# Performance work log

Hardware: AMD Instinct MI355X
Metric: run time of the kernel (lower is better)

## Reference

```python
import jax, jax.numpy as jnp
import numpy as np

B, L, C, H = 256, 200, 4, 128


def setup_inputs() -> dict:
    key = jax.random.key(0)
    ks = jax.random.split(key, 6)
    seqs = jax.random.normal(ks[0], (B, L, C, H), dtype=jnp.float32)
    # valid prefix of random length, padding (True) at the tail
    lengths = jax.random.randint(ks[1], (B,), 1, L + 1)
    timeline_mask = (jnp.arange(L)[None, :] >= lengths[:, None])[:, :, None]  # [B,L,1] bool
    attention_mask = jnp.zeros((L, L), dtype=bool)  # unused by the module
    s = 1.0 / np.sqrt(H)  # torch GRU default init U(-1/sqrt(H), 1/sqrt(H))
    W_ih = jax.random.uniform(ks[2], (C, 3 * H, H), minval=-s, maxval=s, dtype=jnp.float32)
    W_hh = jax.random.uniform(ks[3], (C, 3 * H, H), minval=-s, maxval=s, dtype=jnp.float32)
    b_ih = jax.random.uniform(ks[4], (C, 3 * H), minval=-s, maxval=s, dtype=jnp.float32)
    b_hh = jax.random.uniform(ks[5], (C, 3 * H), minval=-s, maxval=s, dtype=jnp.float32)
    return {"seqs": seqs, "timeline_mask": timeline_mask, "attention_mask": attention_mask,
            "W_ih": W_ih, "W_hh": W_hh, "b_ih": b_ih, "b_hh": b_hh}


def batched_roll(x, shifts):
    # x: [B, L, H]; per-sample circular shift along time (torch.roll semantics)
    Ldim = x.shape[1]
    idx = (jnp.arange(Ldim)[None, :] - shifts[:, None]) % Ldim  # [B, L]
    return jnp.take_along_axis(x, idx[:, :, None], axis=1)


def gru(x, W_ih, W_hh, b_ih, b_hh):
    # single-layer batch_first GRU, h0 = 0 (torch nn.GRU math)
    xp = jnp.einsum('blh,gh->blg', x, W_ih) + b_ih  # [B, L, 3H] input projections
    Hd = W_hh.shape[1]

    def step(h, xt):
        gh = h @ W_hh.T + b_hh
        i_r, i_z, i_n = jnp.split(xt, 3, axis=-1)
        h_r, h_z, h_n = jnp.split(gh, 3, axis=-1)
        r = jax.nn.sigmoid(i_r + h_r)
        z = jax.nn.sigmoid(i_z + h_z)
        n = jnp.tanh(i_n + r * h_n)
        h_new = (1.0 - z) * n + z * h
        return h_new, h_new

    h0 = jnp.zeros((x.shape[0], Hd), x.dtype)
    _, ys = jax.lax.scan(step, h0, jnp.swapaxes(xp, 0, 1))  # scan over time
    return jnp.swapaxes(ys, 0, 1)  # [B, L, H]


def reference(seqs, timeline_mask, attention_mask, W_ih, W_hh, b_ih, b_hh):
    mask = timeline_mask[:, :, 0]                 # [B, L] True = pad
    length = jnp.sum(~mask, axis=1)               # count of valid steps
    zero_length = jnp.sum(mask, axis=1)           # count of padded steps
    outs = []
    for i in range(seqs.shape[2]):                # loop over C experts (distinct weights)
        x = batched_roll(seqs[:, :, i, :], length)
        y = gru(x, W_ih[i], W_hh[i], b_ih[i], b_hh[i])
        y = batched_roll(y, zero_length)
        y = jnp.where(timeline_mask, 0.0, y)      # masked_fill(timeline_mask, 0.0)
        outs.append(y)
    return jnp.stack(outs, axis=0)  # [C, B, L, H] (list of experts in the original)
```

## Files before the change

### kernel.cpp

```cpp
#include <hip/hip_runtime.h>
#include <hip/hip_bf16.h>

#define BB 256
#define LL 200
#define CC 4
#define HH 128
#define G3 384

typedef short bf16x8 __attribute__((ext_vector_type(8)));
typedef float f32x4 __attribute__((ext_vector_type(4)));

#define MFMA16(a, b, c) __builtin_amdgcn_mfma_f32_16x16x32_bf16((a), (b), (c), 0, 0, 0)

__device__ __forceinline__ short bf16_rne(float x) {
    union { float f; unsigned u; } v; v.f = x;
    unsigned r = v.u + 0x7FFFu + ((v.u >> 16) & 1u);
    return (short)(r >> 16);
}
__device__ __forceinline__ float rcp_(float x) { return __builtin_amdgcn_rcpf(x); }
__device__ __forceinline__ float sigm_(float x) { return rcp_(1.0f + __expf(-x)); }
__device__ __forceinline__ float tanhf_(float x) { return 2.0f * rcp_(1.0f + __expf(-2.0f * x)) - 1.0f; }

__device__ __forceinline__ unsigned cvtpk(float lo, float hi) {
    unsigned r;
    asm("v_cvt_pk_bf16_f32 %0, %1, %2" : "=v"(r) : "v"(lo), "v"(hi));
    return r;
}
__device__ __forceinline__ uint2 pack4(float4 v) {
    uint2 p;
    p.x = cvtpk(v.x, v.y);
    p.y = cvtpk(v.z, v.w);
    return p;
}

__global__ void compute_lens_kernel(const unsigned char* __restrict__ mask8,
                                    int* __restrict__ lens) {
    __shared__ int bad;
    int b = threadIdx.x;
    if (b == 0) bad = 0;
    __syncthreads();
    int cnt8 = 0, prev = 0, mono = 1;
    for (int t = 0; t < LL; ++t) {
        int v = mask8[b * LL + t] ? 1 : 0;
        cnt8 += (v == 0);
        if (v < prev) mono = 0;
        prev = v;
    }
    if (!mono) atomicAdd(&bad, 1);
    __syncthreads();
    int len;
    if (bad == 0) {
        len = cnt8;
    } else {
        const int* m32 = (const int*)mask8;
        int c = 0;
        for (int t = 0; t < LL; ++t) c += (m32[b * LL + t] == 0);
        len = c;
    }
    if (len < 1) len = 1;
    if (len > LL) len = LL;
    lens[b] = len;
}

__global__ void wsplit_kernel(const float* __restrict__ Wih, const float* __restrict__ Whh,
                              short* __restrict__ wih_hi, short* __restrict__ whh_hi) {
    int i = blockIdx.x * 256 + threadIdx.x;
    wih_hi[i] = bf16_rne(Wih[i]);
    whh_hi[i] = bf16_rne(Whh[i]);
}

__global__ __launch_bounds__(512, 2) void gru_fused_kernel(
    const float* __restrict__ seqs,
    const int*   __restrict__ lens,
    const short* __restrict__ wih_hi,
    const short* __restrict__ whh_hi,
    const float* __restrict__ b_ih,
    const float* __restrict__ b_hh,
    float*       __restrict__ out)
{
    const int bt = blockIdx.x;
    const int c  = blockIdx.y;
    const int bbase = bt * 16;
    const int tid = threadIdx.x;
    const int w = tid >> 6;
    const int l = tid & 63;
    const int l15 = l & 15, g = l >> 4;

    __shared__ __align__(16) short hA[2][4][512];
    __shared__ __align__(16) short xs[2][4][512];

    bf16x8 BH[3][4], WI[3][4];
    #pragma unroll
    for (int q = 0; q < 3; ++q) {
        const int NT = q * 8 + w;
        #pragma unroll
        for (int ks = 0; ks < 4; ++ks) {
            size_t off = (size_t)(c * G3 + NT * 16 + l15) * HH + ks * 32 + g * 8;
            BH[q][ks] = *(const bf16x8*)(whh_hi + off);
            WI[q][ks] = *(const bf16x8*)(wih_hi + off);
        }
    }

    const int col0 = w * 16 + l15;
    const int ksw = w >> 1;
    const int hwbase = (((w & 1) * 2 + (l15 >> 3)) * 16 + g * 4) * 8 + (l15 & 7);

    const int bsl = tid >> 5;
    const int k0s = (tid & 31) * 4;
    const int ksx = k0s >> 5;
    const int xwbase = ((((k0s >> 3) & 3) * 16 + bsl) * 8 + (k0s & 7));
    const int lenS = lens[bbase + bsl];
    const float* srow0 = seqs + ((size_t)(bbase + bsl) * LL * CC + c) * HH + k0s;
    int ts0 = LL - lenS;
    int ts1 = ts0 + 1; if (ts1 >= LL) ts1 -= LL;
    float4 xr0 = *(const float4*)(srow0 + (size_t)ts0 * (CC * HH));
    float4 xr1 = *(const float4*)(srow0 + (size_t)ts1 * (CC * HH));
    int txs = ts1 + 1; if (txs >= LL) txs -= LL;
    const float* xptr = srow0 + (size_t)txs * (CC * HH);
    const ptrdiff_t xstep = CC * HH;
    const ptrdiff_t xwrap = (ptrdiff_t)(LL - 1) * CC * HH;

    const float bRs = b_hh[c * G3 + col0]       + b_ih[c * G3 + col0];
    const float bZs = b_hh[c * G3 + 128 + col0] + b_ih[c * G3 + 128 + col0];
    const float bHN = b_hh[c * G3 + 256 + col0];
    const float bIN = b_ih[c * G3 + 256 + col0];
    const f32x4 cZZ  = (f32x4){0.f, 0.f, 0.f, 0.f};
    const f32x4 cHN4 = (f32x4){bHN, bHN, bHN, bHN};
    const f32x4 cR4  = (f32x4){bRs, bRs, bRs, bRs};
    const f32x4 cZ4  = (f32x4){bZs, bZs, bZs, bZs};
    const f32x4 cN4  = (f32x4){bIN, bIN, bIN, bIN};

    int lenr[4], tcur[4];
    float* optr[4];
    #pragma unroll
    for (int r = 0; r < 4; ++r) {
        lenr[r] = lens[bbase + g * 4 + r];
        tcur[r] = LL - lenr[r];
        optr[r] = out + ((size_t)(c * BB + bbase + g * 4 + r) * LL + tcur[r]) * HH + col0;
    }
    const ptrdiff_t owrap = (ptrdiff_t)(LL - 1) * HH;
    float hold[4] = { 0.f, 0.f, 0.f, 0.f };

    for (int i = tid; i < 1024; i += 512) ((int*)hA[0])[i] = 0;

    *(uint2*)&xs[0][ksx][xwbase] = pack4(xr0);
    *(uint2*)&xs[1][ksx][xwbase] = pack4(xr1);
    __syncthreads();

    f32x4 xacc[3];
    {
        bf16x8 xh0 = *(const bf16x8*)&xs[0][0][l * 8];
        xacc[0] = MFMA16(xh0, WI[0][0], cR4);
        xacc[1] = MFMA16(xh0, WI[1][0], cZ4);
        xacc[2] = MFMA16(xh0, WI[2][0], cN4);
        #pragma unroll
        for (int ks = 1; ks < 4; ++ks) {
            bf16x8 xh = *(const bf16x8*)&xs[0][ks][l * 8];
            #pragma unroll
            for (int q = 0; q < 3; ++q)
                xacc[q] = MFMA16(xh, WI[q][ks], xacc[q]);
        }
    }
    float4 xraw = *(const float4*)xptr;
    txs = (txs + 1 == LL) ? 0 : txs + 1;
    xptr = (txs == 0) ? xptr - xwrap : xptr + xstep;

    __syncthreads();

#define STEP_BODY(HB, HN)                                                      \
    {                                                                          \
        f32x4 racc[3];                                                         \
        {                                                                      \
            bf16x8 ah0 = *(const bf16x8*)&hA[HB][0][l * 8];                    \
            racc[0] = MFMA16(ah0, BH[0][0], cZZ);                              \
            racc[1] = MFMA16(ah0, BH[1][0], cZZ);                              \
            racc[2] = MFMA16(ah0, BH[2][0], cHN4);                             \
            _Pragma("unroll")                                                  \
            for (int ks = 1; ks < 4; ++ks) {                                   \
                bf16x8 ah = *(const bf16x8*)&hA[HB][ks][l * 8];                \
                _Pragma("unroll")                                              \
                for (int q = 0; q < 3; ++q)                                    \
                    racc[q] = MFMA16(ah, BH[q][ks], racc[q]);                  \
            }                                                                  \
        }                                                                      \
        float hnew[4];                                                         \
        _Pragma("unroll")                                                      \
        for (int r = 0; r < 4; ++r) {                                          \
            float gr = sigm_(racc[0][r] + xacc[0][r]);                         \
            float gz = sigm_(racc[1][r] + xacc[1][r]);                         \
            float gn = tanhf_(xacc[2][r] + gr * racc[2][r]);                   \
            float hv = gn + gz * (hold[r] - gn);                               \
            hnew[r] = hv;                                                      \
            hold[r] = hv;                                                      \
        }                                                                      \
        {                                                                      \
            unsigned pk01 = cvtpk(hold[0], hold[1]);                           \
            unsigned pk23 = cvtpk(hold[2], hold[3]);                           \
            hA[HN][ksw][hwbase]      = (short)(pk01 & 0xffffu);                \
            hA[HN][ksw][hwbase + 8]  = (short)(pk01 >> 16);                    \
            hA[HN][ksw][hwbase + 16] = (short)(pk23 & 0xffffu);                \
            hA[HN][ksw][hwbase + 24] = (short)(pk23 >> 16);                    \
        }                                                                      \
        _Pragma("unroll")                                                      \
        for (int r = 0; r < 4; ++r) {                                          \
            int t = tcur[r];                                                   \
            *optr[r] = (t < lenr[r]) ? hnew[r] : 0.0f;                         \
            int wrapped = (t + 1 == LL);                                       \
            tcur[r] = wrapped ? 0 : t + 1;                                     \
            optr[r] = wrapped ? optr[r] - owrap : optr[r] + HH;                \
        }                                                                      \
        {                                                                      \
            bf16x8 xh0 = *(const bf16x8*)&xs[HN][0][l * 8];                    \
            xacc[0] = MFMA16(xh0, WI[0][0], cR4);                              \
            xacc[1] = MFMA16(xh0, WI[1][0], cZ4);                              \
            xacc[2] = MFMA16(xh0, WI[2][0], cN4);                              \
            _Pragma("unroll")                                                  \
            for (int ks = 1; ks < 4; ++ks) {                                   \
                bf16x8 xh = *(const bf16x8*)&xs[HN][ks][l * 8];                \
                _Pragma("unroll")                                              \
                for (int q = 0; q < 3; ++q)                                    \
                    xacc[q] = MFMA16(xh, WI[q][ks], xacc[q]);                  \
            }                                                                  \
        }                                                                      \
        *(uint2*)&xs[HB][ksx][xwbase] = pack4(xraw);                           \
        xraw = *(const float4*)xptr;                                           \
        txs = (txs + 1 == LL) ? 0 : txs + 1;                                   \
        xptr = (txs == 0) ? xptr - xwrap : xptr + xstep;                       \
        asm volatile("s_waitcnt lgkmcnt(0)" ::: "memory");                     \
        __builtin_amdgcn_s_barrier();                                          \
        __builtin_amdgcn_sched_barrier(0);                                     \
    }

    for (int si2 = 0; si2 < LL; si2 += 2) {
        STEP_BODY(0, 1)
        STEP_BODY(1, 0)
    }
#undef STEP_BODY
}

extern "C" void kernel_launch(void* const* d_in, const int* in_sizes, int n_in,
                              void* d_out, int out_size, void* d_ws, size_t ws_size,
                              hipStream_t stream) {
    const float* seqs  = (const float*)d_in[0];
    const unsigned char* tmask = (const unsigned char*)d_in[1];
    const float* W_ih  = (const float*)d_in[3];
    const float* W_hh  = (const float*)d_in[4];
    const float* b_ih  = (const float*)d_in[5];
    const float* b_hh  = (const float*)d_in[6];
    float* out = (float*)d_out;

    char* ws = (char*)d_ws;
    int*   lens   = (int*)(ws);
    short* wih_hi = (short*)(ws + 1024);
    short* whh_hi = (short*)(ws + 1024 + 393216);

    compute_lens_kernel<<<1, BB, 0, stream>>>(tmask, lens);
    wsplit_kernel<<<768, 256, 0, stream>>>(W_ih, W_hh, wih_hi, whh_hi);

    gru_fused_kernel<<<dim3(16, CC), 512, 0, stream>>>(
        seqs, lens, wih_hi, whh_hi, b_ih, b_hh, out);
}
```

Measured before the change: 202.7 us.

## Transpose MFMA operands so each lane owns 4 hidden dims, vectorize stores

Swaps the MFMA A/B operands so the accumulator holds 4 consecutive hidden dimensions for one batch row per lane, rather than 4 batch rows for one dimension. The hidden state and inputs are now kept in LDS as row-major [batch][padded 136] arrays. With this layout the per-step hidden write becomes a single 8-byte LDS store instead of four 2-byte stores, and the output write becomes one float4 global store with a single length/pointer state per lane. The intent is fewer LDS and global store instructions and more coalesced output writes, at the cost of a different LDS bank-access pattern for the strided bf16x8 reads.

Result: faster. 179.8 us (-11.3%).

```diff
diff --git a/kernel.cpp b/kernel.cpp
--- a/kernel.cpp
+++ b/kernel.cpp
@@ -6,6 +6,7 @@
 #define CC 4
 #define HH 128
 #define G3 384
+#define XP 136
 
 typedef short bf16x8 __attribute__((ext_vector_type(8)));
 typedef float f32x4 __attribute__((ext_vector_type(4)));
@@ -86,8 +87,8 @@
     const int l = tid & 63;
     const int l15 = l & 15, g = l >> 4;
 
-    __shared__ __align__(16) short hA[2][4][512];
-    __shared__ __align__(16) short xs[2][4][512];
+    __shared__ __align__(16) short hA[2][16][XP];
+    __shared__ __align__(16) short xs[2][16][XP];
 
     bf16x8 BH[3][4], WI[3][4];
     #pragma unroll
@@ -101,14 +102,32 @@
         }
     }
 
-    const int col0 = w * 16 + l15;
-    const int ksw = w >> 1;
-    const int hwbase = (((w & 1) * 2 + (l15 >> 3)) * 16 + g * 4) * 8 + (l15 & 7);
+    const int dim0 = w * 16 + g * 4;
+
+    f32x4 cR4, cZ4, cHN4, cN4;
+    {
+        float4 rh = *(const float4*)(b_hh + c * G3 + dim0);
+        float4 ri = *(const float4*)(b_ih + c * G3 + dim0);
+        float4 zh = *(const float4*)(b_hh + c * G3 + 128 + dim0);
+        float4 zi = *(const float4*)(b_ih + c * G3 + 128 + dim0);
+        float4 nh = *(const float4*)(b_hh + c * G3 + 256 + dim0);
+        float4 ni = *(const float4*)(b_ih + c * G3 + 256 + dim0);
+        cR4  = (f32x4){rh.x + ri.x, rh.y + ri.y, rh.z + ri.z, rh.w + ri.w};
+        cZ4  = (f32x4){zh.x + zi.x, zh.y + zi.y, zh.z + zi.z, zh.w + zi.w};
+        cHN4 = (f32x4){nh.x, nh.y, nh.z, nh.w};
+        cN4  = (f32x4){ni.x, ni.y, ni.z, ni.w};
+    }
+    const f32x4 cZZ = (f32x4){0.f, 0.f, 0.f, 0.f};
+
+    const int bme = bbase + l15;
+    const int lenb = lens[bme];
+    int tcur = LL - lenb;
+    float* optr = out + ((size_t)(c * BB + bme) * LL + tcur) * HH + dim0;
+    const ptrdiff_t owrap = (ptrdiff_t)(LL - 1) * HH;
+    float hold[4] = { 0.f, 0.f, 0.f, 0.f };
 
     const int bsl = tid >> 5;
     const int k0s = (tid & 31) * 4;
-    const int ksx = k0s >> 5;
-    const int xwbase = ((((k0s >> 3) & 3) * 16 + bsl) * 8 + (k0s & 7));
     const int lenS = lens[bbase + bsl];
     const float* srow0 = seqs + ((size_t)(bbase + bsl) * LL * CC + c) * HH + k0s;
     int ts0 = LL - lenS;
@@ -120,45 +139,24 @@
     const ptrdiff_t xstep = CC * HH;
     const ptrdiff_t xwrap = (ptrdiff_t)(LL - 1) * CC * HH;
 
-    const float bRs = b_hh[c * G3 + col0]       + b_ih[c * G3 + col0];
-    const float bZs = b_hh[c * G3 + 128 + col0] + b_ih[c * G3 + 128 + col0];
-    const float bHN = b_hh[c * G3 + 256 + col0];
-    const float bIN = b_ih[c * G3 + 256 + col0];
-    const f32x4 cZZ  = (f32x4){0.f, 0.f, 0.f, 0.f};
-    const f32x4 cHN4 = (f32x4){bHN, bHN, bHN, bHN};
-    const f32x4 cR4  = (f32x4){bRs, bRs, bRs, bRs};
-    const f32x4 cZ4  = (f32x4){bZs, bZs, bZs, bZs};
-    const f32x4 cN4  = (f32x4){bIN, bIN, bIN, bIN};
-
-    int lenr[4], tcur[4];
-    float* optr[4];
-    #pragma unroll
-    for (int r = 0; r < 4; ++r) {
-        lenr[r] = lens[bbase + g * 4 + r];
-        tcur[r] = LL - lenr[r];
-        optr[r] = out + ((size_t)(c * BB + bbase + g * 4 + r) * LL + tcur[r]) * HH + col0;
-    }
-    const ptrdiff_t owrap = (ptrdiff_t)(LL - 1) * HH;
-    float hold[4] = { 0.f, 0.f, 0.f, 0.f };
-
-    for (int i = tid; i < 1024; i += 512) ((int*)hA[0])[i] = 0;
-
-    *(uint2*)&xs[0][ksx][xwbase] = pack4(xr0);
-    *(uint2*)&xs[1][ksx][xwbase] = pack4(xr1);
+    for (int i = tid; i < 16 * XP / 2; i += 512) ((int*)hA[0])[i] = 0;
+
+    *(uint2*)&xs[0][bsl][k0s] = pack4(xr0);
+    *(uint2*)&xs[1][bsl][k0s] = pack4(xr1);
     __syncthreads();
 
     f32x4 xacc[3];
     {
-        bf16x8 xh0 = *(const bf16x8*)&xs[0][0][l * 8];
-        xacc[0] = MFMA16(xh0, WI[0][0], cR4);
-        xacc[1] = MFMA16(xh0, WI[1][0], cZ4);
-        xacc[2] = MFMA16(xh0, WI[2][0], cN4);
+        bf16x8 xb0 = *(const bf16x8*)&xs[0][l15][g * 8];
+        xacc[0] = MFMA16(WI[0][0], xb0, cR4);
+        xacc[1] = MFMA16(WI[1][0], xb0, cZ4);
+        xacc[2] = MFMA16(WI[2][0], xb0, cN4);
         #pragma unroll
         for (int ks = 1; ks < 4; ++ks) {
-            bf16x8 xh = *(const bf16x8*)&xs[0][ks][l * 8];
+            bf16x8 xb = *(const bf16x8*)&xs[0][l15][ks * 32 + g * 8];
             #pragma unroll
             for (int q = 0; q < 3; ++q)
-                xacc[q] = MFMA16(xh, WI[q][ks], xacc[q]);
+                xacc[q] = MFMA16(WI[q][ks], xb, xacc[q]);
         }
     }
     float4 xraw = *(const float4*)xptr;
@@ -171,16 +169,16 @@
     {                                                                          \
         f32x4 racc[3];                                                         \
         {                                                                      \
-            bf16x8 ah0 = *(const bf16x8*)&hA[HB][0][l * 8];                    \
-            racc[0] = MFMA16(ah0, BH[0][0], cZZ);                              \
-            racc[1] = MFMA16(ah0, BH[1][0], cZZ);                              \
-            racc[2] = MFMA16(ah0, BH[2][0], cHN4);                             \
+            bf16x8 hb0 = *(const bf16x8*)&hA[HB][l15][g * 8];                  \
+            racc[0] = MFMA16(BH[0][0], hb0, cZZ);                              \
+            racc[1] = MFMA16(BH[1][0], hb0, cZZ);                              \
+            racc[2] = MFMA16(BH[2][0], hb0, cHN4);                             \
             _Pragma("unroll")                                                  \
             for (int ks = 1; ks < 4; ++ks) {                                   \
-                bf16x8 ah = *(const bf16x8*)&hA[HB][ks][l * 8];                \
+                bf16x8 hbf = *(const bf16x8*)&hA[HB][l15][ks * 32 + g * 8];    \
                 _Pragma("unroll")                                              \
                 for (int q = 0; q < 3; ++q)                                    \
-                    racc[q] = MFMA16(ah, BH[q][ks], racc[q]);                  \
+                    racc[q] = MFMA16(BH[q][ks], hbf, racc[q]);                 \
             }                                                                  \
         }                                                                      \
         float hnew[4];                                                         \
@@ -194,35 +192,37 @@
             hold[r] = hv;                                                      \
         }                                                                      \
         {                                                                      \
-            unsigned pk01 = cvtpk(hold[0], hold[1]);                           \
-            unsigned pk23 = cvtpk(hold[2], hold[3]);                           \
-            hA[HN][ksw][hwbase]      = (short)(pk01 & 0xffffu);                \
-            hA[HN][ksw][hwbase + 8]  = (short)(pk01 >> 16);                    \
-            hA[HN][ksw][hwbase + 16] = (short)(pk23 & 0xffffu);                \
-            hA[HN][ksw][hwbase + 24] = (short)(pk23 >> 16);                    \
-        }                                                                      \
-        _Pragma("unroll")                                                      \
-        for (int r = 0; r < 4; ++r) {                                          \
-            int t = tcur[r];                                                   \
-            *optr[r] = (t < lenr[r]) ? hnew[r] : 0.0f;                         \
-            int wrapped = (t + 1 == LL);                                       \
-            tcur[r] = wrapped ? 0 : t + 1;                                     \
-            optr[r] = wrapped ? optr[r] - owrap : optr[r] + HH;                \
-        }                                                                      \
-        {                                                                      \
-            bf16x8 xh0 = *(const bf16x8*)&xs[HN][0][l * 8];                    \
-            xacc[0] = MFMA16(xh0, WI[0][0], cR4);                              \
-            xacc[1] = MFMA16(xh0, WI[1][0], cZ4);                              \
-            xacc[2] = MFMA16(xh0, WI[2][0], cN4);                              \
+            uint2 pk;                                                          \
+            pk.x = cvtpk(hold[0], hold[1]);                                    \
+            pk.y = cvtpk(hold[2], hold[3]);                                    \
+            *(uint2*)&hA[HN][l15][dim0] = pk;         \
+        }                                                                      \
+        {                                                                      \
+            int valid = tcur < lenb;                                           \
+            float4 ov;                                                         \
+            ov.x = valid ? hnew[0] : 0.0f;                                     \
+            ov.y = valid ? hnew[1] : 0.0f;                                     \
+            ov.z = valid ? hnew[2] : 0.0f;                                     \
+            ov.w = valid ? hnew[3] : 0.0f;                                     \
+            *(float4*)optr = ov;                              \
+            int wrapped = (tcur + 1 == LL);                                    \
+            tcur = wrapped ? 0 : tcur + 1;                                     \
+            optr = wrapped ? optr - owrap : optr + HH;                         \
+        }                                                                      \
+        {                                                                      \
+            bf16x8 xb0 = *(const bf16x8*)&xs[HN][l15][g * 8];                  \
+            xacc[0] = MFMA16(WI[0][0], xb0, cR4);                              \
+            xacc[1] = MFMA16(WI[1][0], xb0, cZ4);                              \
+            xacc[2] = MFMA16(WI[2][0], xb0, cN4);                              \
             _Pragma("unroll")                                                  \
             for (int ks = 1; ks < 4; ++ks) {                                   \
-                bf16x8 xh = *(const bf16x8*)&xs[HN][ks][l * 8];                \
+                bf16x8 xb = *(const bf16x8*)&xs[HN][l15][ks * 32 + g * 8];     \
                 _Pragma("unroll")                                              \
                 for (int q = 0; q < 3; ++q)                                    \
-                    xacc[q] = MFMA16(xh, WI[q][ks], xacc[q]);                  \
+                    xacc[q] = MFMA16(WI[q][ks], xb, xacc[q]);                  \
             }                                                                  \
         }                                                                      \
-        *(uint2*)&xs[HB][ksx][xwbase] = pack4(xraw);                           \
+        *(uint2*)&xs[HB][bsl][k0s] = pack4(xraw);                              \
         xraw = *(const float4*)xptr;                                           \
         txs = (txs + 1 == LL) ? 0 : txs + 1;                                   \
         xptr = (txs == 0) ? xptr - xwrap : xptr + xstep;                       \
```
